# Kernel optimization log

Hardware: AMD Instinct MI355X
Metric: run time of the kernel (lower is better)

The kernel has to match this reference:

```python
import math
import jax, jax.numpy as jnp
import numpy as np

B, D, N, L = 2, 1024, 16, 4096


def setup_inputs() -> dict:
    key = jax.random.key(0)
    kx, k1, k2, k3, k4, k5 = jax.random.split(key, 6)
    x = jax.random.normal(kx, (B, D, L), dtype=jnp.float32)
    alpha = jax.random.normal(k1, (D, N, 1), dtype=jnp.float32) * 0.2
    delta = jax.random.normal(k2, (D, N, 1), dtype=jnp.float32) * 0.2
    freqs = math.log(D) / float(D)
    freqs = jnp.exp(jnp.arange(1, D + 1, dtype=jnp.float32) * -freqs)
    perm = jax.random.permutation(k3, D)
    freqs = jnp.clip(freqs[perm], 1e-06, 1.0 - 1e-06)
    theta = jnp.log(freqs / (1.0 - freqs)).reshape(D, 1, 1)
    gamma_real = jax.random.normal(k4, (D, N), dtype=jnp.float32)
    gamma_imag = jnp.zeros((D, N), dtype=jnp.float32)
    omega = jax.random.truncated_normal(k5, -4.0, 4.0, (D,), dtype=jnp.float32) * 0.25
    return {"x": x, "alpha": alpha, "delta": delta, "theta": theta,
            "gamma_real": gamma_real, "gamma_imag": gamma_imag, "omega": omega}


def reference(x, alpha, delta, theta, gamma_real, gamma_imag, omega):
    # FFT path of ComplexEMA (h_init=None, return_state=False, mask=None).
    Bb, Dd, Ll = x.shape
    Nn = alpha.shape[1]
    scale = 1.0 / math.sqrt(float(Nn))
    x32 = x.astype(jnp.float32)

    # --- coefficients (all fp32) ---
    th = jax.nn.sigmoid(theta.astype(jnp.float32)) * (2.0 * jnp.pi / float(Nn))  # (D,1,1)
    wavelets = jnp.arange(1, Nn + 1, dtype=jnp.float32).reshape(1, Nn, 1)
    phi = (wavelets * th).squeeze(-1)                                            # (D,N) angle of q
    a = jax.nn.sigmoid(alpha.astype(jnp.float32))
    d = jax.nn.sigmoid(delta.astype(jnp.float32))
    p = a.squeeze(-1)                                                            # (D,N)
    mag = (1.0 - a * d).squeeze(-1)                                              # (D,N) = |q| (>0)
    radius = jnp.minimum(mag, 1.0)                                               # clip(max=1)
    # gp = gamma * p with gamma = (gr + i*gi) * scale
    gpr = gamma_real.astype(jnp.float32) * scale * p                             # Re(gp)
    gpi = gamma_imag.astype(jnp.float32) * scale * p                             # Im(gp)

    # --- kernel: k[d,l] = Re( sum_n gp[d,n] * q[d,n]^l ) ---
    j = jnp.arange(Ll, dtype=jnp.float32)                                        # (L,)
    magp = radius[:, :, None] ** j[None, None, :]                                # (D,N,L)
    ang = phi[:, :, None] * j[None, None, :]                                     # (D,N,L)
    kernel = (jnp.einsum('dn,dnl->dl', gpr, magp * jnp.cos(ang))
              - jnp.einsum('dn,dnl->dl', gpi, magp * jnp.sin(ang)))              # (D,L)

    # --- FFT convolution ---
    fft_len = 1 << int(2 * Ll - 1).bit_length()
    X = jnp.fft.rfft(x32, n=fft_len, axis=-1)                                    # (B,D,F)
    K = jnp.fft.rfft(kernel, n=fft_len, axis=-1)                                 # (D,F)
    y = jnp.fft.irfft(X * K[None, :, :], n=fft_len, axis=-1)[..., :Ll]           # (B,D,L)

    residual = x32 * omega.astype(jnp.float32)[None, :, None]
    return (y + residual).astype(x.dtype)
```

## Files before the change

### kernel.cpp

```cpp
#include <hip/hip_runtime.h>
#include <math.h>


#define Bq 2
#define Dq 1024
#define Nq 16
#define Lq 4096
#define STR 68

__global__ __launch_bounds__(64) void cema_kernel(
    const float* __restrict__ x,
    const float* __restrict__ alpha,
    const float* __restrict__ delta,
    const float* __restrict__ theta,
    const float* __restrict__ gmr,
    const float* __restrict__ gmi,
    const float* __restrict__ omg,
    float* __restrict__ out)
{
    __shared__ float xs[64 * STR];
    __shared__ float cqr[Nq], cqi[Nq], cgr[Nq], cgi[Nq], cm64r[Nq], cm64i[Nq];
    __shared__ float comega;

    const int bd   = blockIdx.x;
    const int d    = bd & (Dq - 1);
    const int lane = threadIdx.x;

    const float* xp = x + (size_t)bd * Lq;
    float*       yp = out + (size_t)bd * Lq;

    #pragma unroll
    for (int i = 0; i < Lq / (64 * 4); ++i) {
        int e = i * 256 + lane * 4;
        float4 v = *reinterpret_cast<const float4*>(xp + e);
        int chunk = e >> 6, pos = e & 63;
        *reinterpret_cast<float4*>(&xs[chunk * STR + pos]) = v;
    }

    if (lane < Nq) {
        int n = lane;
        float th  = theta[d];
        float f   = 1.f / (1.f + expf(-th));
        float phi = (float)(n + 1) * f * (float)(2.0 * M_PI / (double)Nq);
        float a   = 1.f / (1.f + expf(-alpha[d * Nq + n]));
        float dd  = 1.f / (1.f + expf(-delta[d * Nq + n]));
        float p   = a;
        float radius = fminf(1.f - a * dd, 1.f);
        float s, c;
        sincosf(phi, &s, &c);
        float qr = radius * c, qi = radius * s;
        cqr[n] = qr; cqi[n] = qi;
        const float scale = 0.25f;
        cgr[n] = gmr[d * Nq + n] * scale * p;
        cgi[n] = gmi[d * Nq + n] * scale * p;
        float mr = qr, mi = qi;
        #pragma unroll
        for (int k = 0; k < 6; ++k) {
            float nr = mr * mr - mi * mi;
            float ni = 2.f * mr * mi;
            mr = nr; mi = ni;
        }
        cm64r[n] = mr; cm64i[n] = mi;
    }
    if (lane == 0) comega = omg[d];
    __syncthreads();

    float qr[Nq], qi[Nq], hr[Nq], hi_[Nq];
    #pragma unroll
    for (int n = 0; n < Nq; ++n) {
        qr[n] = cqr[n]; qi[n] = cqi[n];
        hr[n] = 0.f; hi_[n] = 0.f;
    }

    const float4* xc4 = reinterpret_cast<const float4*>(&xs[lane * STR]);
    {
        float4 cur = xc4[0];
        for (int j = 0; j < 16; ++j) {
            float4 nxt = xc4[(j + 1) & 15];
            #pragma unroll
            for (int u = 0; u < 4; ++u) {
                float xv = (u == 0) ? cur.x : (u == 1) ? cur.y : (u == 2) ? cur.z : cur.w;
                #pragma unroll
                for (int n = 0; n < Nq; ++n) {
                    float nr = fmaf(qr[n], hr[n], fmaf(-qi[n], hi_[n], xv));
                    float ni = fmaf(qr[n], hi_[n], qi[n] * hr[n]);
                    hr[n] = nr; hi_[n] = ni;
                }
            }
            cur = nxt;
        }
    }

    #pragma unroll
    for (int n = 0; n < Nq; ++n) {
        float mr = cm64r[n], mi = cm64i[n];
        float vr = hr[n], vi = hi_[n];
        #pragma unroll
        for (int s = 1; s < 64; s <<= 1) {
            float ur = __shfl_up(vr, s, 64);
            float ui = __shfl_up(vi, s, 64);
            if (lane >= s) {
                vr = fmaf(mr, ur, fmaf(-mi, ui, vr));
                vi = fmaf(mr, ui, fmaf(mi, ur, vi));
            }
            float t2 = mr * mr - mi * mi;
            mi = 2.f * mr * mi;
            mr = t2;
        }
        hr[n] = vr; hi_[n] = vi;
    }
    #pragma unroll
    for (int n = 0; n < Nq; ++n) {
        float cr = __shfl_up(hr[n], 1, 64);
        float ci = __shfl_up(hi_[n], 1, 64);
        hr[n]  = (lane > 0) ? cr : 0.f;
        hi_[n] = (lane > 0) ? ci : 0.f;
    }

    float gpr[Nq], gpi[Nq];
    #pragma unroll
    for (int n = 0; n < Nq; ++n) { gpr[n] = cgr[n]; gpi[n] = cgi[n]; }
    float om = comega;

    float4* xcw4 = reinterpret_cast<float4*>(&xs[lane * STR]);
    {
        float4 cur = xcw4[0];
        for (int j = 0; j < 16; ++j) {
            float4 nxt = xcw4[(j + 1) & 15];
            float y0, y1, y2, y3;
            #pragma unroll
            for (int u = 0; u < 4; ++u) {
                float xv = (u == 0) ? cur.x : (u == 1) ? cur.y : (u == 2) ? cur.z : cur.w;
                float acc = om * xv;
                #pragma unroll
                for (int n = 0; n < Nq; ++n) {
                    float nr = fmaf(qr[n], hr[n], fmaf(-qi[n], hi_[n], xv));
                    float ni = fmaf(qr[n], hi_[n], qi[n] * hr[n]);
                    hr[n] = nr; hi_[n] = ni;
                    acc = fmaf(gpr[n], nr, acc);
                    acc = fmaf(-gpi[n], ni, acc);
                }
                if (u == 0) y0 = acc; else if (u == 1) y1 = acc;
                else if (u == 2) y2 = acc; else y3 = acc;
            }
            xcw4[j] = make_float4(y0, y1, y2, y3);
            cur = nxt;
        }
    }
    __syncthreads();

    #pragma unroll
    for (int i = 0; i < Lq / (64 * 4); ++i) {
        int e = i * 256 + lane * 4;
        int chunk = e >> 6, pos = e & 63;
        float4 v = *reinterpret_cast<const float4*>(&xs[chunk * STR + pos]);
        *reinterpret_cast<float4*>(yp + e) = v;
    }
}

extern "C" void kernel_launch(void* const* d_in, const int* in_sizes, int n_in,
                              void* d_out, int out_size, void* d_ws, size_t ws_size,
                              hipStream_t stream) {
    const float* x     = (const float*)d_in[0];
    const float* alpha = (const float*)d_in[1];
    const float* delta = (const float*)d_in[2];
    const float* theta = (const float*)d_in[3];
    const float* gmr   = (const float*)d_in[4];
    const float* gmi   = (const float*)d_in[5];
    const float* omg   = (const float*)d_in[6];

    dim3 grid(Bq * Dq);
    dim3 block(64);
    cema_kernel<<<grid, block, 0, stream>>>(x, alpha, delta, theta, gmr, gmi, omg,
                                            (float*)d_out);
}
```

Before: 124.7 us.

## Split each sequence across two wavefronts with chunked scan and direct global I/O

Each block now uses 128 threads, each handling a 32-element chunk instead of 64. The chunk-level prefix scan runs per wavefront with precomputed power tables, and the two waves are combined through shared memory. The shared-memory staging of x and y is dropped: each thread reads x directly from global twice and writes the output directly. The output accumulation is also split into four partial sums to shorten the FMA dependency chain. This halves the serial recurrence length per thread, at the cost of uncoalesced strided global accesses, an extra sync, and more cross-wave combine work.

```diff
diff --git a/kernel.cpp b/kernel.cpp
--- a/kernel.cpp
+++ b/kernel.cpp
@@ -6,9 +6,9 @@
 #define Dq 1024
 #define Nq 16
 #define Lq 4096
-#define STR 68
+#define CH 32
 
-__global__ __launch_bounds__(64) void cema_kernel(
+__global__ __launch_bounds__(128, 4) void cema_kernel(
     const float* __restrict__ x,
     const float* __restrict__ alpha,
     const float* __restrict__ delta,
@@ -18,72 +18,63 @@
     const float* __restrict__ omg,
     float* __restrict__ out)
 {
-    __shared__ float xs[64 * STR];
-    __shared__ float cqr[Nq], cqi[Nq], cgr[Nq], cgi[Nq], cm64r[Nq], cm64i[Nq];
-    __shared__ float comega;
+    __shared__ float cqr[Nq], cqi[Nq], cgr[Nq], cgi[Nq];
+    __shared__ float Ms[7][2][Nq];
+    __shared__ float Pbuf[64][2 * Nq + 1];
 
-    const int bd   = blockIdx.x;
-    const int d    = bd & (Dq - 1);
-    const int lane = threadIdx.x;
+    const int bd  = blockIdx.x;
+    const int d   = bd & (Dq - 1);
+    const int t   = threadIdx.x;
+    const int w   = t >> 6;
+    const int lam = t & 63;
 
-    const float* xp = x + (size_t)bd * Lq;
-    float*       yp = out + (size_t)bd * Lq;
+    const float* xg = x   + (size_t)bd * Lq + t * CH;
+    float*       yg = out + (size_t)bd * Lq + t * CH;
 
-    #pragma unroll
-    for (int i = 0; i < Lq / (64 * 4); ++i) {
-        int e = i * 256 + lane * 4;
-        float4 v = *reinterpret_cast<const float4*>(xp + e);
-        int chunk = e >> 6, pos = e & 63;
-        *reinterpret_cast<float4*>(&xs[chunk * STR + pos]) = v;
-    }
-
-    if (lane < Nq) {
-        int n = lane;
+    if (t < Nq) {
+        const int n = t;
         float th  = theta[d];
         float f   = 1.f / (1.f + expf(-th));
-        float phi = (float)(n + 1) * f * (float)(2.0 * M_PI / (double)Nq);
+        float phi = (float)(n + 1) * f * (float)(2.0 * M_PI / 16.0);
         float a   = 1.f / (1.f + expf(-alpha[d * Nq + n]));
         float dd  = 1.f / (1.f + expf(-delta[d * Nq + n]));
-        float p   = a;
         float radius = fminf(1.f - a * dd, 1.f);
         float s, c;
         sincosf(phi, &s, &c);
-        float qr = radius * c, qi = radius * s;
-        cqr[n] = qr; cqi[n] = qi;
-        const float scale = 0.25f;
-        cgr[n] = gmr[d * Nq + n] * scale * p;
-        cgi[n] = gmi[d * Nq + n] * scale * p;
-        float mr = qr, mi = qi;
+        float qrv = radius * c, qiv = radius * s;
+        cqr[n] = qrv; cqi[n] = qiv;
+        cgr[n] = gmr[d * Nq + n] * 0.25f * a;
+        cgi[n] = gmi[d * Nq + n] * 0.25f * a;
+        float mr = qrv, mi = qiv;
         #pragma unroll
-        for (int k = 0; k < 6; ++k) {
-            float nr = mr * mr - mi * mi;
-            float ni = 2.f * mr * mi;
-            mr = nr; mi = ni;
+        for (int k = 0; k < 5; ++k) { float t2 = mr*mr - mi*mi; mi = 2.f*mr*mi; mr = t2; }
+        #pragma unroll
+        for (int k = 0; k < 7; ++k) {
+            Ms[k][0][n] = mr; Ms[k][1][n] = mi;
+            float t2 = mr*mr - mi*mi; mi = 2.f*mr*mi; mr = t2;
         }
-        cm64r[n] = mr; cm64i[n] = mi;
     }
-    if (lane == 0) comega = omg[d];
     __syncthreads();
 
-    float qr[Nq], qi[Nq], hr[Nq], hi_[Nq];
+    float qrr[Nq], qii[Nq], hr[Nq], hi_[Nq];
     #pragma unroll
     for (int n = 0; n < Nq; ++n) {
-        qr[n] = cqr[n]; qi[n] = cqi[n];
+        qrr[n] = cqr[n]; qii[n] = cqi[n];
         hr[n] = 0.f; hi_[n] = 0.f;
     }
 
-    const float4* xc4 = reinterpret_cast<const float4*>(&xs[lane * STR]);
     {
-        float4 cur = xc4[0];
-        for (int j = 0; j < 16; ++j) {
-            float4 nxt = xc4[(j + 1) & 15];
+        float4 cur = *reinterpret_cast<const float4*>(xg);
+        for (int i = 0; i < 8; ++i) {
+            int j = (i < 7) ? (i + 1) : 7;
+            float4 nxt = *reinterpret_cast<const float4*>(xg + 4 * j);
             #pragma unroll
             for (int u = 0; u < 4; ++u) {
-                float xv = (u == 0) ? cur.x : (u == 1) ? cur.y : (u == 2) ? cur.z : cur.w;
+                float xe = (u == 0) ? cur.x : (u == 1) ? cur.y : (u == 2) ? cur.z : cur.w;
                 #pragma unroll
                 for (int n = 0; n < Nq; ++n) {
-                    float nr = fmaf(qr[n], hr[n], fmaf(-qi[n], hi_[n], xv));
-                    float ni = fmaf(qr[n], hi_[n], qi[n] * hr[n]);
+                    float nr = fmaf(qrr[n], hr[n], fmaf(-qii[n], hi_[n], xe));
+                    float ni = fmaf(qrr[n], hi_[n], qii[n] * hr[n]);
                     hr[n] = nr; hi_[n] = ni;
                 }
             }
@@ -92,69 +83,79 @@
     }
 
     #pragma unroll
-    for (int n = 0; n < Nq; ++n) {
-        float mr = cm64r[n], mi = cm64i[n];
-        float vr = hr[n], vi = hi_[n];
+    for (int k = 0; k < 6; ++k) {
+        const int s = 1 << k;
         #pragma unroll
-        for (int s = 1; s < 64; s <<= 1) {
-            float ur = __shfl_up(vr, s, 64);
-            float ui = __shfl_up(vi, s, 64);
-            if (lane >= s) {
-                vr = fmaf(mr, ur, fmaf(-mi, ui, vr));
-                vi = fmaf(mr, ui, fmaf(mi, ur, vi));
-            }
-            float t2 = mr * mr - mi * mi;
-            mi = 2.f * mr * mi;
-            mr = t2;
+        for (int n = 0; n < Nq; ++n) {
+            float mr = Ms[k][0][n], mi = Ms[k][1][n];
+            float ur = __shfl_up(hr[n], s, 64);
+            float ui = __shfl_up(hi_[n], s, 64);
+            float vr = fmaf(mr, ur, fmaf(-mi, ui, hr[n]));
+            float vi = fmaf(mr, ui, fmaf(mi, ur, hi_[n]));
+            bool p = (lam >= s);
+            hr[n]  = p ? vr : hr[n];
+            hi_[n] = p ? vi : hi_[n];
         }
-        hr[n] = vr; hi_[n] = vi;
     }
+
+    if (w == 0) {
+        #pragma unroll
+        for (int n = 0; n < Nq; ++n) {
+            Pbuf[lam][2 * n]     = hr[n];
+            Pbuf[lam][2 * n + 1] = hi_[n];
+        }
+    }
+    __syncthreads();
+    if (w == 1) {
+        #pragma unroll
+        for (int n = 0; n < Nq; ++n) {
+            float mr = Ms[6][0][n], mi = Ms[6][1][n];
+            float ur = Pbuf[lam][2 * n], ui = Pbuf[lam][2 * n + 1];
+            hr[n]  = fmaf(mr, ur, fmaf(-mi, ui, hr[n]));
+            hi_[n] = fmaf(mr, ui, fmaf(mi, ur, hi_[n]));
+        }
+    }
+
     #pragma unroll
     for (int n = 0; n < Nq; ++n) {
         float cr = __shfl_up(hr[n], 1, 64);
         float ci = __shfl_up(hi_[n], 1, 64);
-        hr[n]  = (lane > 0) ? cr : 0.f;
-        hi_[n] = (lane > 0) ? ci : 0.f;
+        float br = 0.f, bi = 0.f;
+        if (w == 1) { br = Pbuf[63][2 * n]; bi = Pbuf[63][2 * n + 1]; }
+        hr[n]  = lam ? cr : br;
+        hi_[n] = lam ? ci : bi;
     }
 
     float gpr[Nq], gpi[Nq];
     #pragma unroll
     for (int n = 0; n < Nq; ++n) { gpr[n] = cgr[n]; gpi[n] = cgi[n]; }
-    float om = comega;
+    const float om = omg[d];
 
-    float4* xcw4 = reinterpret_cast<float4*>(&xs[lane * STR]);
     {
-        float4 cur = xcw4[0];
-        for (int j = 0; j < 16; ++j) {
-            float4 nxt = xcw4[(j + 1) & 15];
-            float y0, y1, y2, y3;
+        float4 cur = *reinterpret_cast<const float4*>(xg);
+        for (int i = 0; i < 8; ++i) {
+            int j = (i < 7) ? (i + 1) : 7;
+            float4 nxt = *reinterpret_cast<const float4*>(xg + 4 * j);
+            float yo[4];
             #pragma unroll
             for (int u = 0; u < 4; ++u) {
-                float xv = (u == 0) ? cur.x : (u == 1) ? cur.y : (u == 2) ? cur.z : cur.w;
-                float acc = om * xv;
+                float xe = (u == 0) ? cur.x : (u == 1) ? cur.y : (u == 2) ? cur.z : cur.w;
+                float f0 = om * xe, f1 = 0.f, f2 = 0.f, f3 = 0.f;
                 #pragma unroll
                 for (int n = 0; n < Nq; ++n) {
-                    float nr = fmaf(qr[n], hr[n], fmaf(-qi[n], hi_[n], xv));
-                    float ni = fmaf(qr[n], hi_[n], qi[n] * hr[n]);
+                    float nr = fmaf(qrr[n], hr[n], fmaf(-qii[n], hi_[n], xe));
+                    float ni = fmaf(qrr[n], hi_[n], qii[n] * hr[n]);
                     hr[n] = nr; hi_[n] = ni;
-                    acc = fmaf(gpr[n], nr, acc);
-                    acc = fmaf(-gpi[n], ni, acc);
+                    if ((n & 3) == 0)      { f0 = fmaf(gpr[n], nr, f0); f0 = fmaf(-gpi[n], ni, f0); }
+                    else if ((n & 3) == 1) { f1 = fmaf(gpr[n], nr, f1); f1 = fmaf(-gpi[n], ni, f1); }
+                    else if ((n & 3) == 2) { f2 = fmaf(gpr[n], nr, f2); f2 = fmaf(-gpi[n], ni, f2); }
+                    else                   { f3 = fmaf(gpr[n], nr, f3); f3 = fmaf(-gpi[n], ni, f3); }
                 }
-                if (u == 0) y0 = acc; else if (u == 1) y1 = acc;
-                else if (u == 2) y2 = acc; else y3 = acc;
+                yo[u] = (f0 + f1) + (f2 + f3);
             }
-            xcw4[j] = make_float4(y0, y1, y2, y3);
+            *reinterpret_cast<float4*>(yg + 4 * i) = make_float4(yo[0], yo[1], yo[2], yo[3]);
             cur = nxt;
         }
-    }
-    __syncthreads();
-
-    #pragma unroll
-    for (int i = 0; i < Lq / (64 * 4); ++i) {
-        int e = i * 256 + lane * 4;
-        int chunk = e >> 6, pos = e & 63;
-        float4 v = *reinterpret_cast<const float4*>(&xs[chunk * STR + pos]);
-        *reinterpret_cast<float4*>(yp + e) = v;
     }
 }
 
@@ -170,7 +171,7 @@
     const float* omg   = (const float*)d_in[6];
 
     dim3 grid(Bq * Dq);
-    dim3 block(64);
+    dim3 block(128);
     cema_kernel<<<grid, block, 0, stream>>>(x, alpha, delta, theta, gmr, gmi, omg,
                                             (float*)d_out);
 }
```

Result: slower. 226.1 us (+81.3%).
